# Kernel tuning notes

Measured on AMD Instinct MI355X. Metric: run time of the kernel, lower is better.

## Reference

```python
import jax, jax.numpy as jnp
import numpy as np

N_NODES = 50000
N_EDGES = 800000
HIDDEN = 64
RES = 0.5  # args.res_layer


def setup_inputs() -> dict:
    key = jax.random.key(0)
    ks = jax.random.split(key, 9)
    s = 0.05  # scale weights to keep exp(att) stable
    return {
        "edge_index": jax.random.randint(ks[0], (2, N_EDGES), 0, N_NODES, dtype=jnp.int32),
        "adj_values": jax.random.uniform(ks[1], (N_EDGES,), dtype=jnp.float32),
        "embeds": jax.random.normal(ks[2], (N_NODES, HIDDEN), dtype=jnp.float32),
        "W1": jax.random.normal(ks[3], (HIDDEN, HIDDEN), dtype=jnp.float32) * s,
        "b1": jax.random.normal(ks[4], (HIDDEN,), dtype=jnp.float32) * s,
        "W2": jax.random.normal(ks[5], (HIDDEN, HIDDEN), dtype=jnp.float32) * s,
        "b2": jax.random.normal(ks[6], (HIDDEN,), dtype=jnp.float32) * s,
        "att_w": jax.random.normal(ks[7], (2 * HIDDEN,), dtype=jnp.float32) * s,
        "att_b": jax.random.normal(ks[8], (1,), dtype=jnp.float32) * s,
    }


def reference(edge_index, adj_values, embeds, W1, b1, W2, b2, att_w, att_b):
    n = embeds.shape[0]
    h = embeds.shape[1]
    row, col = edge_index[0], edge_index[1]
    # per-edge gather + two small linears with ReLU
    f1 = jax.nn.relu(embeds[row] @ W1 + b1)          # [E, h]
    f2 = jax.nn.relu(embeds[col] @ W2 + b2)          # [E, h]
    # attention score = Linear(concat(f1, f2)) -> split weight, avoid concat
    att = f1 @ att_w[:h] + f2 @ att_w[h:] + att_b[0]  # [E]
    exp_att = jnp.exp(att)
    # sparse row-wise softmax denominator via segment sum
    rowsum = jax.ops.segment_sum(exp_att, row, num_segments=n) + 1e-6  # [N]
    values = (exp_att / rowsum[row] + RES * adj_values) / (1.0 + RES)  # [E]
    # SpMM: out[i] = sum_{e: row[e]=i} values[e] * embeds[col[e]]
    out = jax.ops.segment_sum(values[:, None] * embeds[col], row, num_segments=n)  # [N, h]
    return values, out
```

## Files before the change

### kernel.cpp

```cpp
#include <hip/hip_runtime.h>
#include <hip/hip_bf16.h>

#define HID 64
#define RES_F 0.5f
#define SLOTS 64

typedef __attribute__((ext_vector_type(8))) short short8;
typedef __attribute__((ext_vector_type(4))) float f32x4;

__device__ __forceinline__ float lane_bcast_f(float v, int k) {
    return __builtin_bit_cast(float, __builtin_amdgcn_readlane(__builtin_bit_cast(int, v), k));
}
__device__ __forceinline__ int lane_bcast_i(int v, int k) {
    return __builtin_amdgcn_readlane(v, k);
}
__device__ __forceinline__ short f2bf(float x) {
    __hip_bfloat16 h = __float2bfloat16(x);
    return __builtin_bit_cast(short, h);
}

__global__ void __launch_bounds__(256) fused_prep_kernel(
    const float* __restrict__ embeds,
    const float* __restrict__ W1, const float* __restrict__ W2,
    const float* __restrict__ b1, const float* __restrict__ b2,
    const float* __restrict__ att_w, const float* __restrict__ att_b,
    const int* __restrict__ row, const int* __restrict__ col,
    const float* __restrict__ adj,
    int* __restrict__ cursor, int* __restrict__ edata,
    float* __restrict__ g, float* __restrict__ corr,
    __hip_bfloat162* __restrict__ embeds_bf,
    int n, int E, int nodeBlocks, int edgeBlocks)
{
    __shared__ short sW[2 * HID * HID];

    if (blockIdx.x < nodeBlocks) {
        for (int i = threadIdx.x; i < HID * HID; i += blockDim.x) {
            sW[i]             = f2bf(W1[i]);
            sW[HID * HID + i] = f2bf(W2[i]);
        }
        __syncthreads();

        const float ab = att_b[0];
        const int lane = threadIdx.x & 63;
        const int colx = lane & 15;
        const int quad = lane >> 4;

        short8 bfrag[8][2];
        float  sac[8], bc[8];
#pragma unroll
        for (int cb = 0; cb < 8; ++cb) {
            const int jp = cb * 16 + colx;
            const short* w = (jp < HID) ? (sW + jp) : (sW + HID * HID + jp - HID);
#pragma unroll
            for (int kh = 0; kh < 2; ++kh) {
                short8 f;
#pragma unroll
                for (int j = 0; j < 8; ++j) {
                    const int k = kh * 32 + quad * 8 + j;
                    f[j] = w[k * HID];
                }
                bfrag[cb][kh] = f;
            }
            sac[cb] = att_w[jp];
            bc[cb]  = (jp < HID) ? b1[jp] : b2[jp - HID];
        }

        int gwave = (blockIdx.x * blockDim.x + threadIdx.x) >> 6;
        const int nwave = (nodeBlocks * blockDim.x) >> 6;
        const int nbatch = (n + 15) >> 4;

        for (int b = gwave; b < nbatch; b += nwave) {
            const int base = b << 4;
            int mrow = base + colx;
            if (mrow >= n) mrow = n - 1;
            const float* ep = embeds + (size_t)mrow * HID;
            short8 afrag0, afrag1;
#pragma unroll
            for (int j = 0; j < 8; ++j) {
                afrag0[j] = f2bf(ep[quad * 8 + j]);
                afrag1[j] = f2bf(ep[32 + quad * 8 + j]);
            }

            float acc1[4] = {0.f, 0.f, 0.f, 0.f};
            float acc2[4] = {0.f, 0.f, 0.f, 0.f};
#pragma unroll
            for (int cb = 0; cb < 8; ++cb) {
                f32x4 C = {0.f, 0.f, 0.f, 0.f};
                C = __builtin_amdgcn_mfma_f32_16x16x32_bf16(afrag0, bfrag[cb][0], C, 0, 0, 0);
                C = __builtin_amdgcn_mfma_f32_16x16x32_bf16(afrag1, bfrag[cb][1], C, 0, 0, 0);
#pragma unroll
                for (int reg = 0; reg < 4; ++reg) {
                    const float v = fmaxf(C[reg] + bc[cb], 0.f) * sac[cb];
                    if (cb < 4) acc1[reg] += v; else acc2[reg] += v;
                }
            }
#pragma unroll
            for (int reg = 0; reg < 4; ++reg) {
#pragma unroll
                for (int off = 1; off < 16; off <<= 1) {
                    acc1[reg] += __shfl_xor(acc1[reg], off, 64);
                    acc2[reg] += __shfl_xor(acc2[reg], off, 64);
                }
            }
            if (colx == 0) {
#pragma unroll
                for (int reg = 0; reg < 4; ++reg) {
                    const int i = base + quad * 4 + reg;
                    if (i < n) {
                        g[i]    = __expf(acc2[reg]);
                        corr[i] = 1e-6f * __expf(-(acc1[reg] + ab));
                    }
                }
            }
        }
    } else {
        const int tid = (blockIdx.x - nodeBlocks) * blockDim.x + threadIdx.x;
        const int ts  = edgeBlocks * blockDim.x;

        const float2* ef2 = (const float2*)embeds;
        const int npair = n * (HID / 2);
        for (int i = tid; i < npair; i += ts) {
            float2 f = ef2[i];
            __hip_bfloat162 h;
            h.x = __float2bfloat16(f.x);
            h.y = __float2bfloat16(f.y);
            embeds_bf[i] = h;
        }

        for (int e = tid; e < E; e += ts) {
            const int r   = row[e];
            const int c   = col[e];
            const float aj = adj[e];
            const int p   = atomicAdd(&cursor[r], 1);
            if (p < SLOTS) {
                const unsigned aq = (unsigned)(aj * 65535.0f + 0.5f);
                edata[(size_t)r * SLOTS + p] = (int)((unsigned)c | (aq << 16));
            }
        }
    }
}

__global__ void __launch_bounds__(256) spmm_kernel(
    const int* __restrict__ cursor, const int* __restrict__ edata,
    const __hip_bfloat16* __restrict__ embeds_bf,
    const float* __restrict__ g, const float* __restrict__ corr,
    float* __restrict__ invD, float* __restrict__ out, int n)
{
    const float inv = 1.0f / (1.0f + RES_F);
    const int lane = threadIdx.x & 63;
    int r = (blockIdx.x * blockDim.x + threadIdx.x) >> 6;
    const int nwave = (gridDim.x * blockDim.x) >> 6;

    for (; r < n; r += nwave) {
        const int deg = min(cursor[r], SLOTS);
        const bool valid = lane < deg;
        int c = 0;
        float gc = 0.0f, aj = 0.0f;
        if (valid) {
            const unsigned pk = (unsigned)edata[(size_t)r * SLOTS + lane];
            c  = (int)(pk & 0xFFFFu);
            aj = (float)(pk >> 16) * (1.0f / 65535.0f);
            gc = g[c];
        }
        float G = gc;
#pragma unroll
        for (int off = 1; off < 64; off <<= 1)
            G += __shfl_xor(G, off, 64);
        const float invDr = 1.0f / (G + corr[r]);
        if (lane == 0) invD[r] = invDr;
        const float v = valid ? (gc * invDr + RES_F * aj) * inv : 0.0f;

        float acc = 0.0f;
        int j = 0;
        for (; j + 8 <= deg; j += 8) {
            const int   c0 = lane_bcast_i(c, j + 0);
            const int   c1 = lane_bcast_i(c, j + 1);
            const int   c2 = lane_bcast_i(c, j + 2);
            const int   c3 = lane_bcast_i(c, j + 3);
            const int   c4 = lane_bcast_i(c, j + 4);
            const int   c5 = lane_bcast_i(c, j + 5);
            const int   c6 = lane_bcast_i(c, j + 6);
            const int   c7 = lane_bcast_i(c, j + 7);
            const float b0 = __bfloat162float(embeds_bf[c0 * HID + lane]);
            const float b1 = __bfloat162float(embeds_bf[c1 * HID + lane]);
            const float b2 = __bfloat162float(embeds_bf[c2 * HID + lane]);
            const float b3 = __bfloat162float(embeds_bf[c3 * HID + lane]);
            const float b4 = __bfloat162float(embeds_bf[c4 * HID + lane]);
            const float b5 = __bfloat162float(embeds_bf[c5 * HID + lane]);
            const float b6 = __bfloat162float(embeds_bf[c6 * HID + lane]);
            const float b7 = __bfloat162float(embeds_bf[c7 * HID + lane]);
            acc = fmaf(lane_bcast_f(v, j + 0), b0, acc);
            acc = fmaf(lane_bcast_f(v, j + 1), b1, acc);
            acc = fmaf(lane_bcast_f(v, j + 2), b2, acc);
            acc = fmaf(lane_bcast_f(v, j + 3), b3, acc);
            acc = fmaf(lane_bcast_f(v, j + 4), b4, acc);
            acc = fmaf(lane_bcast_f(v, j + 5), b5, acc);
            acc = fmaf(lane_bcast_f(v, j + 6), b6, acc);
            acc = fmaf(lane_bcast_f(v, j + 7), b7, acc);
        }
        for (; j < deg; ++j) {
            const int   cj = lane_bcast_i(c, j);
            const float vj = lane_bcast_f(v, j);
            acc = fmaf(vj, __bfloat162float(embeds_bf[cj * HID + lane]), acc);
        }
        out[r * HID + lane] = acc;
    }
}

__global__ void __launch_bounds__(256) values_kernel(
    const int* __restrict__ row, const int* __restrict__ col,
    const float* __restrict__ adj,
    const float* __restrict__ g, const float* __restrict__ invD,
    float* __restrict__ values, int E)
{
    const int e = blockIdx.x * blockDim.x + threadIdx.x;
    if (e < E) {
        const float inv = 1.0f / (1.0f + RES_F);
        values[e] = (g[col[e]] * invD[row[e]] + RES_F * adj[e]) * inv;
    }
}

extern "C" void kernel_launch(void* const* d_in, const int* in_sizes, int n_in,
                              void* d_out, int out_size, void* d_ws, size_t ws_size,
                              hipStream_t stream)
{
    const int* edge_index = (const int*)d_in[0];
    const float* adj      = (const float*)d_in[1];
    const float* embeds   = (const float*)d_in[2];
    const float* W1       = (const float*)d_in[3];
    const float* b1       = (const float*)d_in[4];
    const float* W2       = (const float*)d_in[5];
    const float* b2       = (const float*)d_in[6];
    const float* att_w    = (const float*)d_in[7];
    const float* att_b    = (const float*)d_in[8];

    const int E = in_sizes[1];
    const int N = in_sizes[2] / HID;

    const int* row = edge_index;
    const int* col = edge_index + E;

    int*   edata  = (int*)d_ws;
    float* g      = (float*)(edata + (size_t)N * SLOTS);
    float* corr   = g + N;
    float* invD   = corr + N;
    int*   cursor = (int*)(invD + N);
    __hip_bfloat16* embeds_bf = (__hip_bfloat16*)(cursor + N);

    float* values = (float*)d_out;
    float* out    = values + E;

    (void)hipMemsetAsync(cursor, 0, (size_t)N * sizeof(int), stream);

    const int nodeBlocks = 512;
    const int edgeBlocks = 3125;
    fused_prep_kernel<<<nodeBlocks + edgeBlocks, 256, 0, stream>>>(
        embeds, W1, W2, b1, b2, att_w, att_b, row, col, adj,
        cursor, edata, g, corr, (__hip_bfloat162*)embeds_bf,
        N, E, nodeBlocks, edgeBlocks);

    spmm_kernel<<<12544, 256, 0, stream>>>(cursor, edata, embeds_bf,
                                           g, corr, invD, out, N);

    values_kernel<<<3125, 256, 0, stream>>>(row, col, adj, g, invD, values, E);
}
```

Measured before the change: 165.2 us.

## Partition edge bucketing and SpMM rows into XCD-local node ranges

Edge-bucketing blocks are split into 8 partitions by block index, so each partition scans all edges but only inserts the ones whose row falls in its node range. The SpMM kernel maps blocks to the same node partitions via blockIdx & 7. The apparent aim is to keep cursor/edata atomics and reads local to one XCD's L2 on the multi-die MI355X. The cost is that every edge's row index is now read 8 times, and the grid sizes were changed to fit the new scheme.

```diff
diff --git a/kernel.cpp b/kernel.cpp
--- a/kernel.cpp
+++ b/kernel.cpp
@@ -4,6 +4,7 @@
 #define HID 64
 #define RES_F 0.5f
 #define SLOTS 64
+#define NPART 8
 
 typedef __attribute__((ext_vector_type(8))) short short8;
 typedef __attribute__((ext_vector_type(4))) float f32x4;
@@ -114,12 +115,13 @@
             }
         }
     } else {
-        const int tid = (blockIdx.x - nodeBlocks) * blockDim.x + threadIdx.x;
+        const int ebid = blockIdx.x - nodeBlocks;
+        const int tid_all = ebid * blockDim.x + threadIdx.x;
         const int ts  = edgeBlocks * blockDim.x;
 
         const float2* ef2 = (const float2*)embeds;
         const int npair = n * (HID / 2);
-        for (int i = tid; i < npair; i += ts) {
+        for (int i = tid_all; i < npair; i += ts) {
             float2 f = ef2[i];
             __hip_bfloat162 h;
             h.x = __float2bfloat16(f.x);
@@ -127,14 +129,21 @@
             embeds_bf[i] = h;
         }
 
-        for (int e = tid; e < E; e += ts) {
-            const int r   = row[e];
-            const int c   = col[e];
-            const float aj = adj[e];
-            const int p   = atomicAdd(&cursor[r], 1);
-            if (p < SLOTS) {
-                const unsigned aq = (unsigned)(aj * 65535.0f + 0.5f);
-                edata[(size_t)r * SLOTS + p] = (int)((unsigned)c | (aq << 16));
+        const int p     = ebid & (NPART - 1);
+        const int sub   = ebid >> 3;
+        const int tpp   = (edgeBlocks >> 3) * blockDim.x;
+        const int prows = (n + NPART - 1) / NPART;
+        const int rlo   = p * prows;
+        for (int e = sub * blockDim.x + threadIdx.x; e < E; e += tpp) {
+            const int r = row[e];
+            if ((unsigned)(r - rlo) < (unsigned)prows) {
+                const int c   = col[e];
+                const float aj = adj[e];
+                const int ps  = atomicAdd(&cursor[r], 1);
+                if (ps < SLOTS) {
+                    const unsigned aq = (unsigned)(aj * 65535.0f + 0.5f);
+                    edata[(size_t)r * SLOTS + ps] = (int)((unsigned)c | (aq << 16));
+                }
             }
         }
     }
@@ -148,10 +157,13 @@
 {
     const float inv = 1.0f / (1.0f + RES_F);
     const int lane = threadIdx.x & 63;
-    int r = (blockIdx.x * blockDim.x + threadIdx.x) >> 6;
-    const int nwave = (gridDim.x * blockDim.x) >> 6;
-
-    for (; r < n; r += nwave) {
+    const int prows = (n + NPART - 1) / NPART;
+    const int p   = blockIdx.x & (NPART - 1);
+    const int wi  = (blockIdx.x >> 3) * (blockDim.x >> 6) + (threadIdx.x >> 6);
+    const int r   = p * prows + wi;
+    const int rhi = min((p + 1) * prows, n);
+
+    if (r < rhi) {
         const int deg = min(cursor[r], SLOTS);
         const bool valid = lane < deg;
         int c = 0;
@@ -253,14 +265,17 @@
     (void)hipMemsetAsync(cursor, 0, (size_t)N * sizeof(int), stream);
 
     const int nodeBlocks = 512;
-    const int edgeBlocks = 3125;
+    const int edgeBlocks = 3200;
     fused_prep_kernel<<<nodeBlocks + edgeBlocks, 256, 0, stream>>>(
         embeds, W1, W2, b1, b2, att_w, att_b, row, col, adj,
         cursor, edata, g, corr, (__hip_bfloat162*)embeds_bf,
         N, E, nodeBlocks, edgeBlocks);
 
-    spmm_kernel<<<12544, 256, 0, stream>>>(cursor, edata, embeds_bf,
-                                           g, corr, invD, out, N);
-
-    values_kernel<<<3125, 256, 0, stream>>>(row, col, adj, g, invD, values, E);
-}
+    const int prows = (N + NPART - 1) / NPART;
+    const int bpp   = (prows + 3) / 4;
+    spmm_kernel<<<bpp * NPART, 256, 0, stream>>>(cursor, edata, embeds_bf,
+                                                 g, corr, invD, out, N);
+
+    values_kernel<<<(E + 255) / 256, 256, 0, stream>>>(row, col, adj, g, invD,
+                                                       values, E);
+}
```

Measured after the change: 168.2 us. Within noise of the previous version (+1.8%).
